# Optimization experiments

Hardware: AMD Instinct MI355X
Metric: run time of the kernel (lower is better)

## Reference

```python
import jax, jax.numpy as jnp
import numpy as np

B, F, C, T, E, K = 4, 32, 4096, 32, 65536, 9


def setup_inputs() -> dict:
    key = jax.random.key(0)
    ks = jax.random.split(key, 6)
    x = jax.random.normal(ks[0], (B, F, C, T), jnp.float32)
    edge_index = jax.random.randint(ks[1], (2, E), 0, C, jnp.int32)
    edge_weight = jax.random.uniform(ks[2], (E,), jnp.float32)
    # GCNConv linear weight (stored as [in, out] for einsum) and bias
    W = jax.random.normal(ks[3], (F, F), jnp.float32) / np.sqrt(F)
    gcn_b = jnp.zeros((F,), jnp.float32)
    # temporal Conv2d weight [out, in, 1, K] and bias
    conv_w = jax.random.normal(ks[4], (F, F, 1, K), jnp.float32) / np.sqrt(F * K)
    conv_b = jnp.zeros((F,), jnp.float32)
    return dict(x=x, edge_index=edge_index, edge_weight=edge_weight,
                W=W, gcn_b=gcn_b, conv_w=conv_w, conv_b=conv_b)


def _instance_norm(y, eps=1e-5):
    # InstanceNorm2d(affine=False): normalize per (batch, channel) over (H, W)
    mu = y.mean(axis=(2, 3), keepdims=True)
    var = ((y - mu) ** 2).mean(axis=(2, 3), keepdims=True)
    return (y - mu) * jax.lax.rsqrt(var + eps)


def reference(x, edge_index, edge_weight, W, gcn_b, conv_w, conv_b):
    b, f_in, c, t = x.shape
    src, dst = edge_index[0], edge_index[1]

    # --- GCNConv (PyG gcn_norm with self-loops, fill value 1) ---
    deg = jnp.ones((c,), x.dtype).at[dst].add(edge_weight)  # self-loop contributes 1
    dis = jax.lax.rsqrt(deg)                                 # deg >= 1 here
    norm = dis[src] * edge_weight * dis[dst]                 # [E]

    # linear transform, vectorized over ALL timesteps at once: [b, c, t, f]
    x_lin = jnp.einsum('bfct,fg->bctg', x, W)

    # gather messages from source nodes, scatter-add to destinations
    msgs = x_lin[:, src] * norm[None, :, None, None]          # [b, E, t, f]
    agg = jax.vmap(lambda m: jax.ops.segment_sum(m, dst, num_segments=c))(msgs)
    agg = agg + x_lin * (dis * dis)[None, :, None, None]      # self-loop term
    gcn_out = (agg + gcn_b).transpose(0, 3, 1, 2)             # [b, f, c, t]

    # --- TCN: IN -> ReLU -> Conv2d(1,K) -> IN -> ReLU (dropout = eval no-op) ---
    y = jax.nn.relu(_instance_norm(gcn_out))
    pad = (conv_w.shape[-1] - 1) // 2
    y = jax.lax.conv_general_dilated(
        y, conv_w, window_strides=(1, 1), padding=[(0, 0), (pad, pad)],
        dimension_numbers=('NCHW', 'OIHW', 'NCHW')) + conv_b[None, :, None, None]
    y = jax.nn.relu(_instance_norm(y))

    # residual is Identity (stride=1, in_filters==out_filters)
    return jax.nn.relu(y + x)
```

## Files before the change

kernel.cpp:

```cpp
#include <hip/hip_runtime.h>
#include <cstddef>

namespace {
constexpr int Bn = 4, Fn = 32, Cn = 4096, Tn = 32, En = 65536, Kw = 9;
constexpr int PLANE = Tn * Fn;
}

typedef __attribute__((ext_vector_type(8))) short bf16x8;
typedef __attribute__((ext_vector_type(4))) float f32x4;

static __device__ __forceinline__ unsigned short f2bf(float f) {
    unsigned int u = __float_as_uint(f);
    unsigned int r = (u + 0x7fffu + ((u >> 16) & 1u)) >> 16;
    return (unsigned short)r;
}
static __device__ __forceinline__ float bflo(unsigned u) { return __uint_as_float(u << 16); }
static __device__ __forceinline__ float bfhi(unsigned u) { return __uint_as_float(u & 0xffff0000u); }

__global__ __launch_bounds__(256) void k_init(float* deg, int* hist, int* cnt,
                                              float* s1, float* q1, float* s2, float* q2) {
    int i = blockIdx.x * 256 + threadIdx.x;
    if (i < Cn) { deg[i] = 1.0f; hist[i] = 0; cnt[i] = 0; }
    if (i < Bn * Fn) { s1[i] = 0.f; q1[i] = 0.f; s2[i] = 0.f; q2[i] = 0.f; }
}

__global__ __launch_bounds__(256) void k_deg(const int* ei, const float* ew, float* deg, int* hist) {
    int e = blockIdx.x * 256 + threadIdx.x;
    int d = ei[En + e];
    atomicAdd(&deg[d], ew[e]);
    atomicAdd(&hist[d], 1);
}

__global__ __launch_bounds__(1024) void k_scan(const int* hist, int* ptr) {
    __shared__ int part[1024];
    int tid = threadIdx.x;
    int v0 = hist[tid*4+0], v1 = hist[tid*4+1], v2 = hist[tid*4+2], v3 = hist[tid*4+3];
    int tot = v0 + v1 + v2 + v3;
    part[tid] = tot;
    __syncthreads();
    for (int off = 1; off < 1024; off <<= 1) {
        int add = (tid >= off) ? part[tid - off] : 0;
        __syncthreads();
        part[tid] += add;
        __syncthreads();
    }
    int run = part[tid] - tot;
    ptr[tid*4+0] = run; run += v0;
    ptr[tid*4+1] = run; run += v1;
    ptr[tid*4+2] = run; run += v2;
    ptr[tid*4+3] = run; run += v3;
    if (tid == 1023) ptr[4096] = run;
}

__global__ __launch_bounds__(256) void k_fill(const int* ei, const float* ew, const float* deg,
                                              const int* ptr, int* cnt, int* csrs, float* csrw) {
    int e = blockIdx.x * 256 + threadIdx.x;
    int s = ei[e];
    int d = ei[En + e];
    float w = rsqrtf(deg[s]) * ew[e] * rsqrtf(deg[d]);
    int pos = ptr[d] + atomicAdd(&cnt[d], 1);
    csrs[pos] = s;
    csrw[pos] = w;
}

__global__ __launch_bounds__(256) void k_xlin(const float* __restrict__ x,
                                              const float* __restrict__ W,
                                              ushort* __restrict__ bufA) {
    __shared__ float wl[Fn * Fn];
    int tid = threadIdx.x;
    ((float4*)wl)[tid] = ((const float4*)W)[tid];
    int b  = blockIdx.x >> 9;
    int c0 = (blockIdx.x & 511) << 3;
    __syncthreads();

    float acc[Fn];
    #pragma unroll
    for (int g = 0; g < Fn; ++g) acc[g] = 0.f;

    const float* xp = x + (size_t)b * Fn * Cn * Tn + (size_t)c0 * Tn + tid;
    #pragma unroll
    for (int f = 0; f < Fn; ++f) {
        float xv = xp[(size_t)f * Cn * Tn];
        #pragma unroll
        for (int g = 0; g < Fn; ++g) acc[g] += xv * wl[f * Fn + g];
    }
    ushort* op = bufA + (size_t)(b * Cn + c0) * PLANE + tid * Fn;
    #pragma unroll
    for (int g8 = 0; g8 < 4; ++g8) {
        uint4 pk;
        pk.x = (unsigned)f2bf(acc[g8*8+0]) | ((unsigned)f2bf(acc[g8*8+1]) << 16);
        pk.y = (unsigned)f2bf(acc[g8*8+2]) | ((unsigned)f2bf(acc[g8*8+3]) << 16);
        pk.z = (unsigned)f2bf(acc[g8*8+4]) | ((unsigned)f2bf(acc[g8*8+5]) << 16);
        pk.w = (unsigned)f2bf(acc[g8*8+6]) | ((unsigned)f2bf(acc[g8*8+7]) << 16);
        ((uint4*)op)[g8] = pk;
    }
}

__global__ __launch_bounds__(256) void k_agg(const ushort* __restrict__ bufA,
                                             const float* __restrict__ deg,
                                             const int* __restrict__ ptr,
                                             const int* __restrict__ csrs,
                                             const float* __restrict__ csrw,
                                             const float* __restrict__ gb,
                                             ushort* __restrict__ bufB,
                                             float* s1, float* q1) {
    __shared__ float ssum[Fn], ssq[Fn];
    int tid = threadIdx.x;
    int tile = blockIdx.x & 7;
    int chunk = blockIdx.x >> 3;
    int b = tile >> 1, half = tile & 1;
    int wv = tid >> 6, l = tid & 63;
    if (tid < Fn) { ssum[tid] = 0.f; ssq[tid] = 0.f; }

    const ushort* base = bufA + (size_t)b * Cn * PLANE + half * 512;
    ushort* obase = bufB + (size_t)b * Cn * PLANE + half * 512;
    int e0 = l * 8;
    int f0 = e0 & 31;
    float gbv[8];
    {
        float4 gA = *(const float4*)(gb + f0);
        float4 gB = *(const float4*)(gb + f0 + 4);
        gbv[0]=gA.x; gbv[1]=gA.y; gbv[2]=gA.z; gbv[3]=gA.w;
        gbv[4]=gB.x; gbv[5]=gB.y; gbv[6]=gB.z; gbv[7]=gB.w;
    }

    float st[8], sq[8];
    #pragma unroll
    for (int jj = 0; jj < 8; ++jj) { st[jj] = 0.f; sq[jj] = 0.f; }

    for (int cc = 0; cc < 2; ++cc) {
        int c = chunk * 8 + wv * 2 + cc;
        float d2 = 1.0f / deg[c];
        uint4 sv = *(const uint4*)(base + (size_t)c * PLANE + e0);
        float a[8];
        a[0] = bflo(sv.x) * d2; a[1] = bfhi(sv.x) * d2;
        a[2] = bflo(sv.y) * d2; a[3] = bfhi(sv.y) * d2;
        a[4] = bflo(sv.z) * d2; a[5] = bfhi(sv.z) * d2;
        a[6] = bflo(sv.w) * d2; a[7] = bfhi(sv.w) * d2;

        int j0 = ptr[c], j1 = ptr[c + 1];
        int j = j0;
        for (; j + 7 < j1; j += 8) {
            int s[8]; float w[8]; uint4 u[8];
            #pragma unroll
            for (int i = 0; i < 8; ++i) { s[i] = csrs[j + i]; w[i] = csrw[j + i]; }
            #pragma unroll
            for (int i = 0; i < 8; ++i)
                u[i] = *(const uint4*)(base + (size_t)s[i] * PLANE + e0);
            #pragma unroll
            for (int i = 0; i < 8; ++i) {
                a[0] += bflo(u[i].x) * w[i]; a[1] += bfhi(u[i].x) * w[i];
                a[2] += bflo(u[i].y) * w[i]; a[3] += bfhi(u[i].y) * w[i];
                a[4] += bflo(u[i].z) * w[i]; a[5] += bfhi(u[i].z) * w[i];
                a[6] += bflo(u[i].w) * w[i]; a[7] += bfhi(u[i].w) * w[i];
            }
        }
        if (j + 3 < j1) {
            int s[4]; float w[4]; uint4 u[4];
            #pragma unroll
            for (int i = 0; i < 4; ++i) { s[i] = csrs[j + i]; w[i] = csrw[j + i]; }
            #pragma unroll
            for (int i = 0; i < 4; ++i)
                u[i] = *(const uint4*)(base + (size_t)s[i] * PLANE + e0);
            #pragma unroll
            for (int i = 0; i < 4; ++i) {
                a[0] += bflo(u[i].x) * w[i]; a[1] += bfhi(u[i].x) * w[i];
                a[2] += bflo(u[i].y) * w[i]; a[3] += bfhi(u[i].y) * w[i];
                a[4] += bflo(u[i].z) * w[i]; a[5] += bfhi(u[i].z) * w[i];
                a[6] += bflo(u[i].w) * w[i]; a[7] += bfhi(u[i].w) * w[i];
            }
            j += 4;
        }
        for (; j < j1; ++j) {
            int s0 = csrs[j];
            float w0 = csrw[j];
            uint4 u0 = *(const uint4*)(base + (size_t)s0 * PLANE + e0);
            a[0] += bflo(u0.x) * w0; a[1] += bfhi(u0.x) * w0;
            a[2] += bflo(u0.y) * w0; a[3] += bfhi(u0.y) * w0;
            a[4] += bflo(u0.z) * w0; a[5] += bfhi(u0.z) * w0;
            a[6] += bflo(u0.w) * w0; a[7] += bfhi(u0.w) * w0;
        }

        uint4 pk;
        #pragma unroll
        for (int jj = 0; jj < 8; ++jj) {
            a[jj] += gbv[jj];
            st[jj] += a[jj]; sq[jj] += a[jj] * a[jj];
        }
        pk.x = (unsigned)f2bf(a[0]) | ((unsigned)f2bf(a[1]) << 16);
        pk.y = (unsigned)f2bf(a[2]) | ((unsigned)f2bf(a[3]) << 16);
        pk.z = (unsigned)f2bf(a[4]) | ((unsigned)f2bf(a[5]) << 16);
        pk.w = (unsigned)f2bf(a[6]) | ((unsigned)f2bf(a[7]) << 16);
        *(uint4*)(obase + (size_t)c * PLANE + e0) = pk;
    }

    #pragma unroll
    for (int jj = 0; jj < 8; ++jj) {
        #pragma unroll
        for (int d = 4; d < 64; d <<= 1) {
            st[jj] += __shfl_xor(st[jj], d);
            sq[jj] += __shfl_xor(sq[jj], d);
        }
    }
    __syncthreads();
    if (l < 4) {
        #pragma unroll
        for (int jj = 0; jj < 8; ++jj) {
            atomicAdd(&ssum[f0 + jj], st[jj]);
            atomicAdd(&ssq[f0 + jj], sq[jj]);
        }
    }
    __syncthreads();
    if (tid < Fn) {
        atomicAdd(&s1[b * Fn + tid], ssum[tid]);
        atomicAdd(&q1[b * Fn + tid], ssq[tid]);
    }
}

__global__ __launch_bounds__(256) void k_wfrag(const float* __restrict__ cw,
                                               ushort* __restrict__ wfrag) {
    int tid = blockIdx.x * 256 + threadIdx.x;
    if (tid >= 2 * 9 * 64) return;
    int l  = tid & 63;
    int k  = (tid >> 6) % 9;
    int nt = tid / 576;
    int o  = nt * 16 + (l & 15);
    int ib = (l >> 4) * 8;
    ushort v[8];
    #pragma unroll
    for (int j = 0; j < 8; ++j) v[j] = f2bf(cw[o * 288 + (ib + j) * 9 + k]);
    uint4 pk;
    pk.x = (unsigned)v[0] | ((unsigned)v[1] << 16);
    pk.y = (unsigned)v[2] | ((unsigned)v[3] << 16);
    pk.z = (unsigned)v[4] | ((unsigned)v[5] << 16);
    pk.w = (unsigned)v[6] | ((unsigned)v[7] << 16);
    ((uint4*)wfrag)[tid] = pk;
}

__global__ __launch_bounds__(256) void k_convm(const ushort* __restrict__ bufB,
                                               const float* __restrict__ s1,
                                               const float* __restrict__ q1,
                                               const ushort* __restrict__ wfrag,
                                               const float* __restrict__ cb,
                                               ushort* __restrict__ bufC,
                                               float* s2, float* q2) {
    __shared__ __align__(16) ushort zbuf[4 * 40 * 72];
    __shared__ float ssum[Fn], ssq[Fn];
    int tid = threadIdx.x;
    int l = tid & 63, w = tid >> 6;
    int b  = blockIdx.x >> 9;
    int c0 = (blockIdx.x & 511) * 8 + w * 2;

    if (tid < Fn) { ssum[tid] = 0.f; ssq[tid] = 0.f; }

    ushort* z = zbuf + w * (40 * 72);
    if (l < 16) {
        #pragma unroll
        for (int p = 0; p < 4; ++p) {
            *(unsigned*)&z[p * 72 + l * 2] = 0u;
            *(unsigned*)&z[(36 + p) * 72 + l * 2] = 0u;
        }
    }

    bf16x8 wf0[9], wf1[9];
    #pragma unroll
    for (int k = 0; k < Kw; ++k) {
        wf0[k] = *(const bf16x8*)(wfrag + ((0 * 9 + k) * 64 + l) * 8);
        wf1[k] = *(const bf16x8*)(wfrag + ((1 * 9 + k) * 64 + l) * 8);
    }
    const float invN = 1.0f / (float)(Cn * Tn);
    float pm[16], pr[16];
    {
        int fb = b * Fn + (l & 1) * 16;
        #pragma unroll
        for (int j = 0; j < 16; ++j) {
            float mu = s1[fb + j] * invN;
            float var = q1[fb + j] * invN - mu * mu;
            float r = rsqrtf(var + 1e-5f);
            pm[j] = -mu * r; pr[j] = r;
        }
    }
    float cbv0 = cb[l & 15], cbv1 = cb[16 + (l & 15)];
    __syncthreads();

    float ss0 = 0.f, ss1 = 0.f, qq0 = 0.f, qq1 = 0.f;
    const ushort* za = z + (l & 15) * 72 + (l >> 4) * 8;

    for (int p = 0; p < 2; ++p) {
        int c = c0 + p;
        const ushort* src = bufB + (size_t)(b * Cn + c) * PLANE + l * 16;
        uint4 i0 = *(const uint4*)(src);
        uint4 i1 = *(const uint4*)(src + 8);
        float iv[16] = { bflo(i0.x), bfhi(i0.x), bflo(i0.y), bfhi(i0.y),
                         bflo(i0.z), bfhi(i0.z), bflo(i0.w), bfhi(i0.w),
                         bflo(i1.x), bfhi(i1.x), bflo(i1.y), bfhi(i1.y),
                         bflo(i1.z), bfhi(i1.z), bflo(i1.w), bfhi(i1.w) };
        ushort tmp[16];
        #pragma unroll
        for (int j = 0; j < 16; ++j)
            tmp[j] = f2bf(fmaxf(0.f, iv[j] * pr[j] + pm[j]));
        {
            int t = l >> 1, h = l & 1;
            ushort* zw = z + (t + 4) * 72 + h * 16;
            uint4 w0, w1;
            w0.x = (unsigned)tmp[0] | ((unsigned)tmp[1] << 16);
            w0.y = (unsigned)tmp[2] | ((unsigned)tmp[3] << 16);
            w0.z = (unsigned)tmp[4] | ((unsigned)tmp[5] << 16);
            w0.w = (unsigned)tmp[6] | ((unsigned)tmp[7] << 16);
            w1.x = (unsigned)tmp[8] | ((unsigned)tmp[9] << 16);
            w1.y = (unsigned)tmp[10] | ((unsigned)tmp[11] << 16);
            w1.z = (unsigned)tmp[12] | ((unsigned)tmp[13] << 16);
            w1.w = (unsigned)tmp[14] | ((unsigned)tmp[15] << 16);
            *(uint4*)(zw) = w0;
            *(uint4*)(zw + 8) = w1;
        }

        f32x4 acc00 = {0,0,0,0}, acc01 = {0,0,0,0}, acc10 = {0,0,0,0}, acc11 = {0,0,0,0};
        #pragma unroll
        for (int k = 0; k < Kw; ++k) {
            bf16x8 a0 = *(const bf16x8*)(za + k * 72);
            acc00 = __builtin_amdgcn_mfma_f32_16x16x32_bf16(a0, wf0[k], acc00, 0, 0, 0);
            acc01 = __builtin_amdgcn_mfma_f32_16x16x32_bf16(a0, wf1[k], acc01, 0, 0, 0);
        }
        #pragma unroll
        for (int k = 0; k < Kw; ++k) {
            bf16x8 a1 = *(const bf16x8*)(za + (16 + k) * 72);
            acc10 = __builtin_amdgcn_mfma_f32_16x16x32_bf16(a1, wf0[k], acc10, 0, 0, 0);
            acc11 = __builtin_amdgcn_mfma_f32_16x16x32_bf16(a1, wf1[k], acc11, 0, 0, 0);
        }

        ushort* dst = bufC + (size_t)(b * Cn + c) * PLANE;
        int col = l & 15, r0 = (l >> 4) * 4;
        #pragma unroll
        for (int r = 0; r < 4; ++r) {
            float v00 = acc00[r] + cbv0;
            float v01 = acc01[r] + cbv1;
            float v10 = acc10[r] + cbv0;
            float v11 = acc11[r] + cbv1;
            dst[(r0 + r) * 32 + col]            = f2bf(v00);
            dst[(r0 + r) * 32 + 16 + col]       = f2bf(v01);
            dst[(16 + r0 + r) * 32 + col]       = f2bf(v10);
            dst[(16 + r0 + r) * 32 + 16 + col]  = f2bf(v11);
            ss0 += v00 + v10; qq0 += v00 * v00 + v10 * v10;
            ss1 += v01 + v11; qq1 += v01 * v01 + v11 * v11;
        }
    }

    ss0 += __shfl_xor(ss0, 16); ss0 += __shfl_xor(ss0, 32);
    qq0 += __shfl_xor(qq0, 16); qq0 += __shfl_xor(qq0, 32);
    ss1 += __shfl_xor(ss1, 16); ss1 += __shfl_xor(ss1, 32);
    qq1 += __shfl_xor(qq1, 16); qq1 += __shfl_xor(qq1, 32);
    if ((l >> 4) == 0) {
        atomicAdd(&ssum[l], ss0);      atomicAdd(&ssq[l], qq0);
        atomicAdd(&ssum[16 + l], ss1); atomicAdd(&ssq[16 + l], qq1);
    }
    __syncthreads();
    if (tid < Fn) {
        atomicAdd(&s2[b * Fn + tid], ssum[tid]);
        atomicAdd(&q2[b * Fn + tid], ssq[tid]);
    }
}

__global__ __launch_bounds__(256) void k_final(const ushort* __restrict__ bufC,
                                               const float* __restrict__ x,
                                               const float* __restrict__ s2,
                                               const float* __restrict__ q2,
                                               float* __restrict__ out) {
    __shared__ float yl[Tn * 33];
    int tid = threadIdx.x;
    int blk = blockIdx.x;
    int b = blk >> 12, c = blk & (Cn - 1);
    {
        uint2 v = ((const uint2*)(bufC + (size_t)(b * Cn + c) * PLANE))[tid];
        int t = tid >> 3, f0 = (tid & 7) * 4;
        yl[t * 33 + f0 + 0] = bflo(v.x);
        yl[t * 33 + f0 + 1] = bfhi(v.x);
        yl[t * 33 + f0 + 2] = bflo(v.y);
        yl[t * 33 + f0 + 3] = bfhi(v.y);
    }
    __syncthreads();
    int f = tid >> 3, tb = (tid & 7) * 4;
    const float invN = 1.0f / (float)(Cn * Tn);
    float mu = s2[b * Fn + f] * invN;
    float var = q2[b * Fn + f] * invN - mu * mu;
    float r = rsqrtf(var + 1e-5f);
    size_t base = ((size_t)(b * Fn + f) * Cn + c) * Tn + tb;
    float4 xv = *(const float4*)(x + base);
    float xx[4] = {xv.x, xv.y, xv.z, xv.w};
    float oo[4];
    #pragma unroll
    for (int j = 0; j < 4; ++j) {
        float y = yl[(tb + j) * 33 + f];
        float yn = fmaxf(0.f, (y - mu) * r);
        oo[j] = fmaxf(0.f, yn + xx[j]);
    }
    *(float4*)(out + base) = make_float4(oo[0], oo[1], oo[2], oo[3]);
}

extern "C" void kernel_launch(void* const* d_in, const int* in_sizes, int n_in,
                              void* d_out, int out_size, void* d_ws, size_t ws_size,
                              hipStream_t stream) {
    const float* x  = (const float*)d_in[0];
    const int*   ei = (const int*)d_in[1];
    const float* ew = (const float*)d_in[2];
    const float* W  = (const float*)d_in[3];
    const float* gb = (const float*)d_in[4];
    const float* cw = (const float*)d_in[5];
    const float* cb = (const float*)d_in[6];
    float* out = (float*)d_out;

    char* p = (char*)d_ws;
    auto alloc = [&](size_t bytes) {
        char* r = p;
        p += (bytes + 255) & ~(size_t)255;
        return r;
    };
    ushort* bufA = (ushort*)alloc(sizeof(ushort) * (size_t)Bn * Cn * PLANE);
    ushort* bufB = (ushort*)alloc(sizeof(ushort) * (size_t)Bn * Cn * PLANE);
    ushort* bufC = (ushort*)alloc(sizeof(ushort) * (size_t)Bn * Cn * PLANE);
    float* deg  = (float*)alloc(sizeof(float) * Cn);
    int*   hist = (int*)alloc(sizeof(int) * Cn);
    int*   cnt  = (int*)alloc(sizeof(int) * Cn);
    int*   ptr  = (int*)alloc(sizeof(int) * (Cn + 1));
    int*   csrs = (int*)alloc(sizeof(int) * En);
    float* csrw = (float*)alloc(sizeof(float) * En);
    float* s1   = (float*)alloc(sizeof(float) * Bn * Fn);
    float* q1   = (float*)alloc(sizeof(float) * Bn * Fn);
    float* s2   = (float*)alloc(sizeof(float) * Bn * Fn);
    float* q2   = (float*)alloc(sizeof(float) * Bn * Fn);
    ushort* wfrag = (ushort*)alloc(sizeof(ushort) * 2 * 9 * 64 * 8);
    if ((size_t)(p - (char*)d_ws) > ws_size) return;

    k_init<<<Cn / 256, 256, 0, stream>>>(deg, hist, cnt, s1, q1, s2, q2);
    k_wfrag<<<5, 256, 0, stream>>>(cw, wfrag);
    k_deg<<<En / 256, 256, 0, stream>>>(ei, ew, deg, hist);
    k_scan<<<1, 1024, 0, stream>>>(hist, ptr);
    k_fill<<<En / 256, 256, 0, stream>>>(ei, ew, deg, ptr, cnt, csrs, csrw);
    k_xlin<<<Bn * (Cn / 8), 256, 0, stream>>>(x, W, bufA);
    k_agg<<<Cn, 256, 0, stream>>>(bufA, deg, ptr, csrs, csrw, gb, bufB, s1, q1);
    k_convm<<<Bn * (Cn / 8), 256, 0, stream>>>(bufB, s1, q1, wfrag, cb, bufC, s2, q2);
    k_final<<<Bn * Cn, 256, 0, stream>>>(bufC, x, s2, q2, out);
}
```

Measured before the change: 179.7 us.

## Fold weight-fragment prep into init; one node per wave in aggregation

The weight-fragment packing kernel is merged into the init kernel, which removes one launch. The aggregation kernel now handles one destination node per wave instead of two, doubling the grid to 8192 blocks for more parallelism and latency hiding. Source indices are made wave-uniform with readfirstlane so address arithmetic can use scalar registers. The output store is nontemporal. The trade-off is more blocks, each paying the shared-memory and atomic reduction overhead, which doubles the atomics to the stats arrays.

```diff
diff --git a/kernel.cpp b/kernel.cpp
--- a/kernel.cpp
+++ b/kernel.cpp
@@ -8,6 +8,7 @@
 
 typedef __attribute__((ext_vector_type(8))) short bf16x8;
 typedef __attribute__((ext_vector_type(4))) float f32x4;
+typedef __attribute__((ext_vector_type(4))) unsigned int u32x4;
 
 static __device__ __forceinline__ unsigned short f2bf(float f) {
     unsigned int u = __float_as_uint(f);
@@ -18,10 +19,28 @@
 static __device__ __forceinline__ float bfhi(unsigned u) { return __uint_as_float(u & 0xffff0000u); }
 
 __global__ __launch_bounds__(256) void k_init(float* deg, int* hist, int* cnt,
-                                              float* s1, float* q1, float* s2, float* q2) {
+                                              float* s1, float* q1, float* s2, float* q2,
+                                              const float* __restrict__ cw,
+                                              ushort* __restrict__ wfrag) {
     int i = blockIdx.x * 256 + threadIdx.x;
     if (i < Cn) { deg[i] = 1.0f; hist[i] = 0; cnt[i] = 0; }
     if (i < Bn * Fn) { s1[i] = 0.f; q1[i] = 0.f; s2[i] = 0.f; q2[i] = 0.f; }
+    if (i < 2 * 9 * 64) {
+        int l  = i & 63;
+        int k  = (i >> 6) % 9;
+        int nt = i / 576;
+        int o  = nt * 16 + (l & 15);
+        int ib = (l >> 4) * 8;
+        ushort v[8];
+        #pragma unroll
+        for (int j = 0; j < 8; ++j) v[j] = f2bf(cw[o * 288 + (ib + j) * 9 + k]);
+        uint4 pk;
+        pk.x = (unsigned)v[0] | ((unsigned)v[1] << 16);
+        pk.y = (unsigned)v[2] | ((unsigned)v[3] << 16);
+        pk.z = (unsigned)v[4] | ((unsigned)v[5] << 16);
+        pk.w = (unsigned)v[6] | ((unsigned)v[7] << 16);
+        ((uint4*)wfrag)[i] = pk;
+    }
 }
 
 __global__ __launch_bounds__(256) void k_deg(const int* ei, const float* ew, float* deg, int* hist) {
@@ -110,6 +129,7 @@
     int chunk = blockIdx.x >> 3;
     int b = tile >> 1, half = tile & 1;
     int wv = tid >> 6, l = tid & 63;
+    int c = chunk * 4 + wv;
     if (tid < Fn) { ssum[tid] = 0.f; ssq[tid] = 0.f; }
 
     const ushort* base = bufA + (size_t)b * Cn * PLANE + half * 512;
@@ -124,75 +144,79 @@
         gbv[4]=gB.x; gbv[5]=gB.y; gbv[6]=gB.z; gbv[7]=gB.w;
     }
 
-    float st[8], sq[8];
-    #pragma unroll
-    for (int jj = 0; jj < 8; ++jj) { st[jj] = 0.f; sq[jj] = 0.f; }
-
-    for (int cc = 0; cc < 2; ++cc) {
-        int c = chunk * 8 + wv * 2 + cc;
+    float a[8];
+    {
         float d2 = 1.0f / deg[c];
         uint4 sv = *(const uint4*)(base + (size_t)c * PLANE + e0);
-        float a[8];
         a[0] = bflo(sv.x) * d2; a[1] = bfhi(sv.x) * d2;
         a[2] = bflo(sv.y) * d2; a[3] = bfhi(sv.y) * d2;
         a[4] = bflo(sv.z) * d2; a[5] = bfhi(sv.z) * d2;
         a[6] = bflo(sv.w) * d2; a[7] = bfhi(sv.w) * d2;
-
-        int j0 = ptr[c], j1 = ptr[c + 1];
-        int j = j0;
-        for (; j + 7 < j1; j += 8) {
-            int s[8]; float w[8]; uint4 u[8];
-            #pragma unroll
-            for (int i = 0; i < 8; ++i) { s[i] = csrs[j + i]; w[i] = csrw[j + i]; }
-            #pragma unroll
-            for (int i = 0; i < 8; ++i)
-                u[i] = *(const uint4*)(base + (size_t)s[i] * PLANE + e0);
-            #pragma unroll
-            for (int i = 0; i < 8; ++i) {
-                a[0] += bflo(u[i].x) * w[i]; a[1] += bfhi(u[i].x) * w[i];
-                a[2] += bflo(u[i].y) * w[i]; a[3] += bfhi(u[i].y) * w[i];
-                a[4] += bflo(u[i].z) * w[i]; a[5] += bfhi(u[i].z) * w[i];
-                a[6] += bflo(u[i].w) * w[i]; a[7] += bfhi(u[i].w) * w[i];
-            }
-        }
-        if (j + 3 < j1) {
-            int s[4]; float w[4]; uint4 u[4];
-            #pragma unroll
-            for (int i = 0; i < 4; ++i) { s[i] = csrs[j + i]; w[i] = csrw[j + i]; }
-            #pragma unroll
-            for (int i = 0; i < 4; ++i)
-                u[i] = *(const uint4*)(base + (size_t)s[i] * PLANE + e0);
-            #pragma unroll
-            for (int i = 0; i < 4; ++i) {
-                a[0] += bflo(u[i].x) * w[i]; a[1] += bfhi(u[i].x) * w[i];
-                a[2] += bflo(u[i].y) * w[i]; a[3] += bfhi(u[i].y) * w[i];
-                a[4] += bflo(u[i].z) * w[i]; a[5] += bfhi(u[i].z) * w[i];
-                a[6] += bflo(u[i].w) * w[i]; a[7] += bfhi(u[i].w) * w[i];
-            }
-            j += 4;
-        }
-        for (; j < j1; ++j) {
-            int s0 = csrs[j];
-            float w0 = csrw[j];
-            uint4 u0 = *(const uint4*)(base + (size_t)s0 * PLANE + e0);
-            a[0] += bflo(u0.x) * w0; a[1] += bfhi(u0.x) * w0;
-            a[2] += bflo(u0.y) * w0; a[3] += bfhi(u0.y) * w0;
-            a[4] += bflo(u0.z) * w0; a[5] += bfhi(u0.z) * w0;
-            a[6] += bflo(u0.w) * w0; a[7] += bfhi(u0.w) * w0;
-        }
-
-        uint4 pk;
-        #pragma unroll
-        for (int jj = 0; jj < 8; ++jj) {
-            a[jj] += gbv[jj];
-            st[jj] += a[jj]; sq[jj] += a[jj] * a[jj];
-        }
-        pk.x = (unsigned)f2bf(a[0]) | ((unsigned)f2bf(a[1]) << 16);
-        pk.y = (unsigned)f2bf(a[2]) | ((unsigned)f2bf(a[3]) << 16);
-        pk.z = (unsigned)f2bf(a[4]) | ((unsigned)f2bf(a[5]) << 16);
-        pk.w = (unsigned)f2bf(a[6]) | ((unsigned)f2bf(a[7]) << 16);
-        *(uint4*)(obase + (size_t)c * PLANE + e0) = pk;
-    }
+    }
+
+#define ACC8(U, W) { \
+        a[0] += bflo((U).x) * (W); a[1] += bfhi((U).x) * (W); \
+        a[2] += bflo((U).y) * (W); a[3] += bfhi((U).y) * (W); \
+        a[4] += bflo((U).z) * (W); a[5] += bfhi((U).z) * (W); \
+        a[6] += bflo((U).w) * (W); a[7] += bfhi((U).w) * (W); }
+
+    int j0 = ptr[c], j1 = ptr[c + 1];
+    int j = j0;
+    for (; j + 7 < j1; j += 8) {
+        int s0 = __builtin_amdgcn_readfirstlane(csrs[j + 0]);
+        int s1v= __builtin_amdgcn_readfirstlane(csrs[j + 1]);
+        int s2 = __builtin_amdgcn_readfirstlane(csrs[j + 2]);
+        int s3 = __builtin_amdgcn_readfirstlane(csrs[j + 3]);
+        int s4 = __builtin_amdgcn_readfirstlane(csrs[j + 4]);
+        int s5 = __builtin_amdgcn_readfirstlane(csrs[j + 5]);
+        int s6 = __builtin_amdgcn_readfirstlane(csrs[j + 6]);
+        int s7 = __builtin_amdgcn_readfirstlane(csrs[j + 7]);
+        float w0 = csrw[j+0], w1 = csrw[j+1], w2 = csrw[j+2], w3 = csrw[j+3];
+        float w4 = csrw[j+4], w5 = csrw[j+5], w6 = csrw[j+6], w7 = csrw[j+7];
+        uint4 u0 = *(const uint4*)(base + (size_t)s0  * PLANE + e0);
+        uint4 u1 = *(const uint4*)(base + (size_t)s1v * PLANE + e0);
+        uint4 u2 = *(const uint4*)(base + (size_t)s2  * PLANE + e0);
+        uint4 u3 = *(const uint4*)(base + (size_t)s3  * PLANE + e0);
+        uint4 u4 = *(const uint4*)(base + (size_t)s4  * PLANE + e0);
+        uint4 u5 = *(const uint4*)(base + (size_t)s5  * PLANE + e0);
+        uint4 u6 = *(const uint4*)(base + (size_t)s6  * PLANE + e0);
+        uint4 u7 = *(const uint4*)(base + (size_t)s7  * PLANE + e0);
+        ACC8(u0, w0); ACC8(u1, w1); ACC8(u2, w2); ACC8(u3, w3);
+        ACC8(u4, w4); ACC8(u5, w5); ACC8(u6, w6); ACC8(u7, w7);
+    }
+    if (j + 3 < j1) {
+        int s0 = __builtin_amdgcn_readfirstlane(csrs[j + 0]);
+        int s1v= __builtin_amdgcn_readfirstlane(csrs[j + 1]);
+        int s2 = __builtin_amdgcn_readfirstlane(csrs[j + 2]);
+        int s3 = __builtin_amdgcn_readfirstlane(csrs[j + 3]);
+        float w0 = csrw[j+0], w1 = csrw[j+1], w2 = csrw[j+2], w3 = csrw[j+3];
+        uint4 u0 = *(const uint4*)(base + (size_t)s0  * PLANE + e0);
+        uint4 u1 = *(const uint4*)(base + (size_t)s1v * PLANE + e0);
+        uint4 u2 = *(const uint4*)(base + (size_t)s2  * PLANE + e0);
+        uint4 u3 = *(const uint4*)(base + (size_t)s3  * PLANE + e0);
+        ACC8(u0, w0); ACC8(u1, w1); ACC8(u2, w2); ACC8(u3, w3);
+        j += 4;
+    }
+    for (; j < j1; ++j) {
+        int s0 = __builtin_amdgcn_readfirstlane(csrs[j]);
+        float w0 = csrw[j];
+        uint4 u0 = *(const uint4*)(base + (size_t)s0 * PLANE + e0);
+        ACC8(u0, w0);
+    }
+#undef ACC8
+
+    float st[8], sq[8];
+    u32x4 pk;
+    #pragma unroll
+    for (int jj = 0; jj < 8; ++jj) {
+        a[jj] += gbv[jj];
+        st[jj] = a[jj]; sq[jj] = a[jj] * a[jj];
+    }
+    pk.x = (unsigned)f2bf(a[0]) | ((unsigned)f2bf(a[1]) << 16);
+    pk.y = (unsigned)f2bf(a[2]) | ((unsigned)f2bf(a[3]) << 16);
+    pk.z = (unsigned)f2bf(a[4]) | ((unsigned)f2bf(a[5]) << 16);
+    pk.w = (unsigned)f2bf(a[6]) | ((unsigned)f2bf(a[7]) << 16);
+    __builtin_nontemporal_store(pk, (u32x4*)(obase + (size_t)c * PLANE + e0));
 
     #pragma unroll
     for (int jj = 0; jj < 8; ++jj) {
@@ -215,26 +239,6 @@
         atomicAdd(&s1[b * Fn + tid], ssum[tid]);
         atomicAdd(&q1[b * Fn + tid], ssq[tid]);
     }
-}
-
-__global__ __launch_bounds__(256) void k_wfrag(const float* __restrict__ cw,
-                                               ushort* __restrict__ wfrag) {
-    int tid = blockIdx.x * 256 + threadIdx.x;
-    if (tid >= 2 * 9 * 64) return;
-    int l  = tid & 63;
-    int k  = (tid >> 6) % 9;
-    int nt = tid / 576;
-    int o  = nt * 16 + (l & 15);
-    int ib = (l >> 4) * 8;
-    ushort v[8];
-    #pragma unroll
-    for (int j = 0; j < 8; ++j) v[j] = f2bf(cw[o * 288 + (ib + j) * 9 + k]);
-    uint4 pk;
-    pk.x = (unsigned)v[0] | ((unsigned)v[1] << 16);
-    pk.y = (unsigned)v[2] | ((unsigned)v[3] << 16);
-    pk.z = (unsigned)v[4] | ((unsigned)v[5] << 16);
-    pk.w = (unsigned)v[6] | ((unsigned)v[7] << 16);
-    ((uint4*)wfrag)[tid] = pk;
 }
 
 __global__ __launch_bounds__(256) void k_convm(const ushort* __restrict__ bufB,
@@ -431,13 +435,12 @@
     ushort* wfrag = (ushort*)alloc(sizeof(ushort) * 2 * 9 * 64 * 8);
     if ((size_t)(p - (char*)d_ws) > ws_size) return;
 
-    k_init<<<Cn / 256, 256, 0, stream>>>(deg, hist, cnt, s1, q1, s2, q2);
-    k_wfrag<<<5, 256, 0, stream>>>(cw, wfrag);
+    k_init<<<Cn / 256, 256, 0, stream>>>(deg, hist, cnt, s1, q1, s2, q2, cw, wfrag);
     k_deg<<<En / 256, 256, 0, stream>>>(ei, ew, deg, hist);
     k_scan<<<1, 1024, 0, stream>>>(hist, ptr);
     k_fill<<<En / 256, 256, 0, stream>>>(ei, ew, deg, ptr, cnt, csrs, csrw);
     k_xlin<<<Bn * (Cn / 8), 256, 0, stream>>>(x, W, bufA);
-    k_agg<<<Cn, 256, 0, stream>>>(bufA, deg, ptr, csrs, csrw, gb, bufB, s1, q1);
+    k_agg<<<Cn * 2, 256, 0, stream>>>(bufA, deg, ptr, csrs, csrw, gb, bufB, s1, q1);
     k_convm<<<Bn * (Cn / 8), 256, 0, stream>>>(bufB, s1, q1, wfrag, cb, bufC, s2, q2);
     k_final<<<Bn * Cn, 256, 0, stream>>>(bufC, x, s2, q2, out);
 }
```

New measurement: 196.0 us. +9.0%, slower.
